# Kernel optimization log

Measured on AMD Instinct MI355X. Metric: run time of the kernel, lower is better.

## Reference

```python
import jax, jax.numpy as jnp
import numpy as np

DIM = 1024
HEADS = 16
HEAD_DIM = DIM // HEADS
FEAT = 256
B, N = 4, 4096


def setup_inputs() -> dict:
    key = jax.random.key(0)
    ks = jax.random.split(key, 10)
    s = 1.0 / np.sqrt(DIM)
    return {
        "x": jax.random.normal(ks[0], (B, N, DIM), jnp.float32),
        "Wq": jax.random.normal(ks[1], (DIM, DIM), jnp.float32) * s,
        "bq": jnp.zeros((DIM,), jnp.float32),
        "Wk": jax.random.normal(ks[2], (DIM, DIM), jnp.float32) * s,
        "bk": jnp.zeros((DIM,), jnp.float32),
        "Wv": jax.random.normal(ks[3], (DIM, DIM), jnp.float32) * s,
        "bv": jnp.zeros((DIM,), jnp.float32),
        "Wo": jax.random.normal(ks[4], (DIM, DIM), jnp.float32) * s,
        "bo": jnp.zeros((DIM,), jnp.float32),
        "random_features": jax.random.normal(ks[5], (HEAD_DIM, FEAT), jnp.float32) / np.sqrt(FEAT),
    }


def reference(x, Wq, bq, Wk, bk, Wv, bv, Wo, bo, random_features):
    Bsz, Nlen, C = x.shape
    # linear projections, reshape to (B, N, H, head_dim)
    q = (x @ Wq + bq).reshape(Bsz, Nlen, HEADS, HEAD_DIM)
    k = (x @ Wk + bk).reshape(Bsz, Nlen, HEADS, HEAD_DIM)
    v = (x @ Wv + bv).reshape(Bsz, Nlen, HEADS, HEAD_DIM)
    # positive feature map: elu(x)+1
    q = jax.nn.elu(q) + 1.0
    k = jax.nn.elu(k) + 1.0
    # random-feature projection (B, N, H, F)
    q = jnp.einsum('bnhd,df->bnhf', q, random_features)
    k = jnp.einsum('bnhd,df->bnhf', k, random_features)
    # kernelized linear attention (no normalization, non-causal as in source)
    kv = jnp.einsum('bnhf,bnhd->bhfd', k, v)          # (B, H, F, head_dim)
    out = jnp.einsum('bnhf,bhfd->bnhd', q, kv)        # (B, N, H, head_dim)
    out = out.reshape(Bsz, Nlen, C)
    return out @ Wo + bo
```

## Files before the change

### kernel.cpp

```cpp
#include <hip/hip_runtime.h>
#include <hip/hip_bf16.h>
#include <cstdint>
#include <cstddef>

using bf16 = __hip_bfloat16;
typedef __attribute__((ext_vector_type(8))) __bf16 bf16x8;
typedef __attribute__((ext_vector_type(4))) float f32x4;

typedef const __attribute__((address_space(1))) void CGV;
typedef __attribute__((address_space(3))) void LDSV;

__device__ __forceinline__ void gload_lds16(const void* g, void* l) {
    __builtin_amdgcn_global_load_lds((CGV*)g, (LDSV*)l, 16, 0, 0);
}

__device__ __forceinline__ float bits2f(unsigned short u) {
    return __uint_as_float(((unsigned)u) << 16);
}
__device__ __forceinline__ unsigned short f2bits(float f) {
    return __builtin_bit_cast(unsigned short, __float2bfloat16(f));
}

__global__ void cast_f32_bf16(const float4* __restrict__ in, ushort4* __restrict__ out, int n4) {
    int i = blockIdx.x * 256 + threadIdx.x;
    if (i < n4) {
        float4 f = in[i];
        ushort4 u;
        u.x = f2bits(f.x); u.y = f2bits(f.y); u.z = f2bits(f.z); u.w = f2bits(f.w);
        out[i] = u;
    }
}

__global__ void transpose_cast(const float* __restrict__ A, const float* __restrict__ B,
                               const float* __restrict__ C, bf16* __restrict__ Wt3) {
    const float* W = (blockIdx.z == 0) ? A : (blockIdx.z == 1) ? B : C;
    bf16* O = Wt3 + (size_t)blockIdx.z * (1024 * 1024);
    __shared__ float tile[32][33];
    int x = blockIdx.x * 32 + threadIdx.x;
    int y0 = blockIdx.y * 32;
    for (int i = threadIdx.y; i < 32; i += 8)
        tile[i][threadIdx.x] = W[(size_t)(y0 + i) * 1024 + x];
    __syncthreads();
    int xo = blockIdx.y * 32 + threadIdx.x;
    int yo = blockIdx.x * 32;
    for (int i = threadIdx.y; i < 32; i += 8)
        O[(size_t)(yo + i) * 1024 + xo] = __float2bfloat16(tile[threadIdx.x][i]);
}

__global__ void g_kernel(const float* __restrict__ RF, float* __restrict__ G) {
    int o = blockIdx.x * 256 + threadIdx.x;
    int i = o >> 6, j = o & 63;
    const float4* a = (const float4*)(RF + (size_t)i * 256);
    const float4* b = (const float4*)(RF + (size_t)j * 256);
    float s = 0.f;
    for (int f = 0; f < 64; f++) {
        float4 x = a[f], y = b[f];
        s += x.x * y.x + x.y * y.y + x.z * y.z + x.w * y.w;
    }
    G[o] = s;
}

__global__ __launch_bounds__(256, 2) void gemm_qkv(
    const bf16* __restrict__ X, const bf16* __restrict__ Wt3,
    const float* __restrict__ bq, const float* __restrict__ bk, const float* __restrict__ bv,
    bf16* __restrict__ Qo, bf16* __restrict__ Ko, bf16* __restrict__ Vo)
{
    __shared__ bf16 As[128 * 64];
    __shared__ bf16 Bs[128 * 64];
    const int z = blockIdx.z;
    const int lid = blockIdx.x + (blockIdx.y << 3);
    const int xcd = lid & 7, seq = lid >> 3;
    const int m0 = (xcd * 16 + (seq >> 3)) * 128;
    const int n0 = (seq & 7) * 128;
    const int tid = threadIdx.x;
    const int w = tid >> 6, lane = tid & 63;
    const int lr = lane >> 3, lc = lane & 7;
    const int sc = lc ^ lr;
    const bf16* Wt = Wt3 + (size_t)z * (1024 * 1024);

    const bf16* ag = X  + (size_t)(m0 + w * 32 + lr) * 1024 + sc * 8;
    const bf16* bg = Wt + (size_t)(n0 + w * 32 + lr) * 1024 + sc * 8;
    bf16* al = As + (w * 32) * 64;
    bf16* bl = Bs + (w * 32) * 64;

    f32x4 acc[4][4];
#pragma unroll
    for (int i = 0; i < 4; i++)
#pragma unroll
        for (int j = 0; j < 4; j++) acc[i][j] = (f32x4){0.f, 0.f, 0.f, 0.f};

    const int lm = lane & 15, quad = lane >> 4;
    const int x0 = (quad ^ (lm & 7)) * 8;
    const int x1 = ((quad + 4) ^ (lm & 7)) * 8;
    const bf16* Ab = As + ((w >> 1) * 64 + lm) * 64;
    const bf16* Bb = Bs + ((w & 1) * 64 + lm) * 64;

    for (int k0 = 0; k0 < 1024; k0 += 64) {
#pragma unroll
        for (int j = 0; j < 4; j++) {
            gload_lds16(ag + (size_t)j * 8 * 1024 + k0, al + j * 8 * 64);
            gload_lds16(bg + (size_t)j * 8 * 1024 + k0, bl + j * 8 * 64);
        }
        __syncthreads();
#pragma unroll
        for (int kk = 0; kk < 2; kk++) {
            const int xo = kk ? x1 : x0;
            bf16x8 a[4], b[4];
#pragma unroll
            for (int i = 0; i < 4; i++) a[i] = *(const bf16x8*)(Ab + i * 16 * 64 + xo);
#pragma unroll
            for (int i = 0; i < 4; i++) b[i] = *(const bf16x8*)(Bb + i * 16 * 64 + xo);
#pragma unroll
            for (int mi = 0; mi < 4; mi++)
#pragma unroll
                for (int ni = 0; ni < 4; ni++)
                    acc[mi][ni] = __builtin_amdgcn_mfma_f32_16x16x32_bf16(
                        a[mi], b[ni], acc[mi][ni], 0, 0, 0);
        }
        __syncthreads();
    }

    const int wr = (w >> 1) * 64, wc = (w & 1) * 64;
    if (z == 0) {
#pragma unroll
        for (int ni = 0; ni < 4; ni++) {
            int col = n0 + wc + ni * 16 + lm;
            float bs = bq[col];
#pragma unroll
            for (int mi = 0; mi < 4; mi++) {
                int row0 = m0 + wr + mi * 16 + quad * 4;
#pragma unroll
                for (int r = 0; r < 4; r++) {
                    float v = acc[mi][ni][r] + bs;
                    v = (v > 0.f) ? (v + 1.f) : __expf(v);
                    Qo[(size_t)(row0 + r) * 1024 + col] = __float2bfloat16(v);
                }
            }
        }
    } else {
        const float* bias = (z == 1) ? bk : bv;
        bf16* Out = (z == 1) ? Ko : Vo;
#pragma unroll
        for (int ni = 0; ni < 4; ni++) {
            int col = n0 + wc + ni * 16 + lm;
            float bs = bias[col];
            int h = col >> 6, d = col & 63;
#pragma unroll
            for (int mi = 0; mi < 4; mi++) {
                int row0 = m0 + wr + mi * 16 + quad * 4;
#pragma unroll
                for (int r = 0; r < 4; r++) {
                    int row = row0 + r;
                    int b = row >> 12, n = row & 4095;
                    float v = acc[mi][ni][r] + bs;
                    if (z == 1) v = (v > 0.f) ? (v + 1.f) : __expf(v);
                    Out[(((size_t)(b * 16 + h) * 4096 + n) << 6) + d] = __float2bfloat16(v);
                }
            }
        }
    }
}

__global__ __launch_bounds__(256, 2) void s_kernel(const bf16* __restrict__ Kp,
                                                   const bf16* __restrict__ Vp,
                                                   float* __restrict__ Spart)
{
    __shared__ bf16 Ks[256 * 64];
    __shared__ bf16 Vs[256 * 64];
    const int bh = blockIdx.x, sp = blockIdx.y;
    const int t = threadIdx.x;
    const int w = t >> 6, lane = t & 63;
    const int eb = (t >> 4) * 4, db = (t & 15) * 4;
    const size_t base = ((size_t)bh * 4096 + sp * 512) * 64;

    float acc[4][4];
#pragma unroll
    for (int i = 0; i < 4; i++)
#pragma unroll
        for (int j = 0; j < 4; j++) acc[i][j] = 0.f;

    const unsigned short* ks = (const unsigned short*)Ks;
    const unsigned short* vs = (const unsigned short*)Vs;

    for (int tile = 0; tile < 2; tile++) {
        const bf16* kg = Kp + base + tile * (256 * 64) + (size_t)w * 4096 + lane * 8;
        const bf16* vg = Vp + base + tile * (256 * 64) + (size_t)w * 4096 + lane * 8;
#pragma unroll
        for (int r = 0; r < 8; r++) {
            gload_lds16(kg + r * 512, Ks + w * 4096 + r * 512);
            gload_lds16(vg + r * 512, Vs + w * 4096 + r * 512);
        }
        __syncthreads();
#pragma unroll 4
        for (int n = 0; n < 256; n++) {
            ushort4 ku = *(const ushort4*)(ks + n * 64 + eb);
            ushort4 vu = *(const ushort4*)(vs + n * 64 + db);
            float kf[4] = {bits2f(ku.x), bits2f(ku.y), bits2f(ku.z), bits2f(ku.w)};
            float vf[4] = {bits2f(vu.x), bits2f(vu.y), bits2f(vu.z), bits2f(vu.w)};
#pragma unroll
            for (int i = 0; i < 4; i++)
#pragma unroll
                for (int j = 0; j < 4; j++) acc[i][j] += kf[i] * vf[j];
        }
        __syncthreads();
    }

    float* spb = Spart + ((size_t)sp * 64 + bh) * 4096;
#pragma unroll
    for (int i = 0; i < 4; i++)
#pragma unroll
        for (int j = 0; j < 4; j++) spb[(eb + i) * 64 + db + j] = acc[i][j];
}

__global__ void reduce_s(const float* __restrict__ Spart, float* __restrict__ S) {
    int bh = blockIdx.x, t = threadIdx.x;
    for (int v = 0; v < 4; v++) {
        int idx = v * 1024 + t * 4;
        float4 a = {0.f, 0.f, 0.f, 0.f};
        for (int s2 = 0; s2 < 8; s2++) {
            float4 p = *(const float4*)&Spart[((size_t)s2 * 64 + bh) * 4096 + idx];
            a.x += p.x; a.y += p.y; a.z += p.z; a.w += p.w;
        }
        *(float4*)&S[(size_t)bh * 4096 + idx] = a;
    }
}

__global__ __launch_bounds__(256) void m_kernel(const float* __restrict__ S,
                                                const float* __restrict__ G,
                                                float* __restrict__ M)
{
    __shared__ float Sl[4096];
    int bh = blockIdx.x, t = threadIdx.x;
    for (int i = t; i < 4096; i += 256) Sl[i] = S[(size_t)bh * 4096 + i];
    __syncthreads();
    int e = t >> 2, d0 = (t & 3) * 16;
    float acc[16];
#pragma unroll
    for (int j = 0; j < 16; j++) acc[j] = 0.f;
    for (int ep = 0; ep < 64; ep++) {
        float g = G[e * 64 + ep];
#pragma unroll
        for (int j = 0; j < 16; j++) acc[j] += g * Sl[ep * 64 + d0 + j];
    }
#pragma unroll
    for (int j = 0; j < 16; j++) M[(size_t)bh * 4096 + e * 64 + d0 + j] = acc[j];
}

__global__ __launch_bounds__(256) void fold_kernel(const float* __restrict__ M,
                                                   const float* __restrict__ Wo,
                                                   bf16* __restrict__ Wo2t)
{
    int x = blockIdx.x;
    int b = x >> 6, h = (x >> 2) & 15, cb = x & 3;
    __shared__ float Ml[4096];
    int t = threadIdx.x;
    for (int i = t; i < 4096; i += 256) {
        int e = i >> 6, d = i & 63;
        Ml[d * 64 + e] = M[((size_t)b * 16 + h) * 4096 + i];
    }
    __syncthreads();
    int c = cb * 256 + t;
    float acc[64];
#pragma unroll
    for (int e = 0; e < 64; e++) acc[e] = 0.f;
    for (int d = 0; d < 64; d++) {
        float wo = Wo[(size_t)(h * 64 + d) * 1024 + c];
#pragma unroll
        for (int e = 0; e < 64; e++) acc[e] += Ml[d * 64 + e] * wo;
    }
    unsigned* outp = (unsigned*)(Wo2t + ((size_t)b * 1024 + c) * 1024 + h * 64);
#pragma unroll
    for (int e = 0; e < 64; e += 2) {
        unsigned lo = f2bits(acc[e]);
        unsigned hi = f2bits(acc[e + 1]);
        outp[e >> 1] = lo | (hi << 16);
    }
}

__global__ __launch_bounds__(256, 2) void gemm_out(
    const bf16* __restrict__ Qp, const bf16* __restrict__ Wo2t,
    const float* __restrict__ bo, float* __restrict__ Out)
{
    __shared__ bf16 As[128 * 64];
    __shared__ bf16 Bs[128 * 64];
    const int lid = blockIdx.x + (blockIdx.y << 3);
    const int xcd = lid & 7, seq = lid >> 3;
    const int m0 = (xcd * 16 + (seq >> 3)) * 128;
    const int n0 = (seq & 7) * 128;
    const int tid = threadIdx.x;
    const int w = tid >> 6, lane = tid & 63;
    const int lr = lane >> 3, lc = lane & 7;
    const int sc = lc ^ lr;
    const bf16* Wt = Wo2t + (size_t)(m0 >> 12) * (1024 * 1024);

    const bf16* ag = Qp + (size_t)(m0 + w * 32 + lr) * 1024 + sc * 8;
    const bf16* bg = Wt + (size_t)(n0 + w * 32 + lr) * 1024 + sc * 8;
    bf16* al = As + (w * 32) * 64;
    bf16* bl = Bs + (w * 32) * 64;

    f32x4 acc[4][4];
#pragma unroll
    for (int i = 0; i < 4; i++)
#pragma unroll
        for (int j = 0; j < 4; j++) acc[i][j] = (f32x4){0.f, 0.f, 0.f, 0.f};

    const int lm = lane & 15, quad = lane >> 4;
    const int x0 = (quad ^ (lm & 7)) * 8;
    const int x1 = ((quad + 4) ^ (lm & 7)) * 8;
    const bf16* Ab = As + ((w >> 1) * 64 + lm) * 64;
    const bf16* Bb = Bs + ((w & 1) * 64 + lm) * 64;

    for (int k0 = 0; k0 < 1024; k0 += 64) {
#pragma unroll
        for (int j = 0; j < 4; j++) {
            gload_lds16(ag + (size_t)j * 8 * 1024 + k0, al + j * 8 * 64);
            gload_lds16(bg + (size_t)j * 8 * 1024 + k0, bl + j * 8 * 64);
        }
        __syncthreads();
#pragma unroll
        for (int kk = 0; kk < 2; kk++) {
            const int xo = kk ? x1 : x0;
            bf16x8 a[4], b[4];
#pragma unroll
            for (int i = 0; i < 4; i++) a[i] = *(const bf16x8*)(Ab + i * 16 * 64 + xo);
#pragma unroll
            for (int i = 0; i < 4; i++) b[i] = *(const bf16x8*)(Bb + i * 16 * 64 + xo);
#pragma unroll
            for (int mi = 0; mi < 4; mi++)
#pragma unroll
                for (int ni = 0; ni < 4; ni++)
                    acc[mi][ni] = __builtin_amdgcn_mfma_f32_16x16x32_bf16(
                        a[mi], b[ni], acc[mi][ni], 0, 0, 0);
        }
        __syncthreads();
    }

    const int wr = (w >> 1) * 64, wc = (w & 1) * 64;
#pragma unroll
    for (int ni = 0; ni < 4; ni++) {
        int col = n0 + wc + ni * 16 + lm;
        float bs = bo[col];
#pragma unroll
        for (int mi = 0; mi < 4; mi++) {
            int row0 = m0 + wr + mi * 16 + quad * 4;
#pragma unroll
            for (int r = 0; r < 4; r++)
                Out[(size_t)(row0 + r) * 1024 + col] = acc[mi][ni][r] + bs;
        }
    }
}

extern "C" void kernel_launch(void* const* d_in, const int* in_sizes, int n_in,
                              void* d_out, int out_size, void* d_ws, size_t ws_size,
                              hipStream_t stream) {
    const float* x  = (const float*)d_in[0];
    const float* Wq = (const float*)d_in[1];
    const float* bq = (const float*)d_in[2];
    const float* Wk = (const float*)d_in[3];
    const float* bk = (const float*)d_in[4];
    const float* Wv = (const float*)d_in[5];
    const float* bv = (const float*)d_in[6];
    const float* Wo = (const float*)d_in[7];
    const float* bo = (const float*)d_in[8];
    const float* RF = (const float*)d_in[9];
    float* out = (float*)d_out;

    char* ws = (char*)d_ws;
    bf16*  Xb    = (bf16*) (ws);
    bf16*  Qp    = (bf16*) (ws + ((size_t)32  << 20));
    bf16*  Kp    = (bf16*) (ws + ((size_t)64  << 20));
    bf16*  Vp    = (bf16*) (ws + ((size_t)96  << 20));
    bf16*  Wt3   = (bf16*) (ws + ((size_t)128 << 20));
    bf16*  Wo2t  = (bf16*) (ws + ((size_t)134 << 20));
    float* Spart = (float*)(ws + ((size_t)142 << 20));
    float* S     = (float*)(ws + ((size_t)150 << 20));
    float* Mm    = (float*)(ws + ((size_t)151 << 20));
    float* G     = (float*)(ws + ((size_t)152 << 20));

    cast_f32_bf16<<<16384, 256, 0, stream>>>((const float4*)x, (ushort4*)Xb, 4194304);
    transpose_cast<<<dim3(32, 32, 3), dim3(32, 8), 0, stream>>>(Wq, Wk, Wv, Wt3);
    g_kernel<<<16, 256, 0, stream>>>(RF, G);
    gemm_qkv<<<dim3(8, 128, 3), 256, 0, stream>>>(Xb, Wt3, bq, bk, bv, Qp, Kp, Vp);
    s_kernel<<<dim3(64, 8), 256, 0, stream>>>(Kp, Vp, Spart);
    reduce_s<<<64, 256, 0, stream>>>(Spart, S);
    m_kernel<<<64, 256, 0, stream>>>(S, G, Mm);
    fold_kernel<<<256, 256, 0, stream>>>(Mm, Wo, Wo2t);
    gemm_out<<<dim3(8, 128), 256, 0, stream>>>(Qp, Wo2t, bo, out);
}
```

Baseline: 394.4 us.

## Merge prep kernels and fuse reduce/M/fold; raise GEMM occupancy hint

Three small preprocessing kernels (input cast, weight transpose-cast, RF Gram) are combined into one launch dispatched by block index. The split-S reduction, M computation and Wo fold are fused into one kernel, so each of its blocks redoes the Spart reduction and G multiply that the separate kernels did once. This removes launch gaps and intermediate global round-trips at the cost of redundant work. The QKV and output GEMM launch bounds change from 2 to 4 blocks per CU, which may constrain registers.

```diff
diff --git a/kernel.cpp b/kernel.cpp
--- a/kernel.cpp
+++ b/kernel.cpp
@@ -21,46 +21,53 @@
     return __builtin_bit_cast(unsigned short, __float2bfloat16(f));
 }
 
-__global__ void cast_f32_bf16(const float4* __restrict__ in, ushort4* __restrict__ out, int n4) {
-    int i = blockIdx.x * 256 + threadIdx.x;
-    if (i < n4) {
-        float4 f = in[i];
+__global__ __launch_bounds__(256) void prep_kernel(
+    const float4* __restrict__ x4, ushort4* __restrict__ Xb4,
+    const float* __restrict__ Wq, const float* __restrict__ Wk,
+    const float* __restrict__ Wv, bf16* __restrict__ Wt3,
+    const float* __restrict__ RF, float* __restrict__ G)
+{
+    const int bi = blockIdx.x;
+    const int t = threadIdx.x;
+    if (bi < 16384) {
+        int i = bi * 256 + t;
+        float4 f = x4[i];
         ushort4 u;
         u.x = f2bits(f.x); u.y = f2bits(f.y); u.z = f2bits(f.z); u.w = f2bits(f.w);
-        out[i] = u;
-    }
-}
-
-__global__ void transpose_cast(const float* __restrict__ A, const float* __restrict__ B,
-                               const float* __restrict__ C, bf16* __restrict__ Wt3) {
-    const float* W = (blockIdx.z == 0) ? A : (blockIdx.z == 1) ? B : C;
-    bf16* O = Wt3 + (size_t)blockIdx.z * (1024 * 1024);
-    __shared__ float tile[32][33];
-    int x = blockIdx.x * 32 + threadIdx.x;
-    int y0 = blockIdx.y * 32;
-    for (int i = threadIdx.y; i < 32; i += 8)
-        tile[i][threadIdx.x] = W[(size_t)(y0 + i) * 1024 + x];
-    __syncthreads();
-    int xo = blockIdx.y * 32 + threadIdx.x;
-    int yo = blockIdx.x * 32;
-    for (int i = threadIdx.y; i < 32; i += 8)
-        O[(size_t)(yo + i) * 1024 + xo] = __float2bfloat16(tile[threadIdx.x][i]);
-}
-
-__global__ void g_kernel(const float* __restrict__ RF, float* __restrict__ G) {
-    int o = blockIdx.x * 256 + threadIdx.x;
-    int i = o >> 6, j = o & 63;
-    const float4* a = (const float4*)(RF + (size_t)i * 256);
-    const float4* b = (const float4*)(RF + (size_t)j * 256);
-    float s = 0.f;
-    for (int f = 0; f < 64; f++) {
-        float4 x = a[f], y = b[f];
-        s += x.x * y.x + x.y * y.y + x.z * y.z + x.w * y.w;
-    }
-    G[o] = s;
-}
-
-__global__ __launch_bounds__(256, 2) void gemm_qkv(
+        Xb4[i] = u;
+    } else if (bi < 19456) {
+        int rem = bi - 16384;
+        int z = rem >> 10;
+        int r2 = rem & 1023;
+        int bx = r2 & 31, by = r2 >> 5;
+        const float* W = (z == 0) ? Wq : (z == 1) ? Wk : Wv;
+        bf16* O = Wt3 + (size_t)z * (1024 * 1024);
+        __shared__ float tile[32][33];
+        int tx = t & 31, ty = t >> 5;
+        int xg = bx * 32 + tx;
+        int y0 = by * 32;
+        for (int i = ty; i < 32; i += 8)
+            tile[i][tx] = W[(size_t)(y0 + i) * 1024 + xg];
+        __syncthreads();
+        int xo = by * 32 + tx;
+        int yo = bx * 32;
+        for (int i = ty; i < 32; i += 8)
+            O[(size_t)(yo + i) * 1024 + xo] = __float2bfloat16(tile[tx][i]);
+    } else {
+        int o = (bi - 19456) * 256 + t;
+        int i = o >> 6, j = o & 63;
+        const float4* a = (const float4*)(RF + (size_t)i * 256);
+        const float4* b = (const float4*)(RF + (size_t)j * 256);
+        float s = 0.f;
+        for (int f = 0; f < 64; f++) {
+            float4 xx = a[f], yy = b[f];
+            s += xx.x * yy.x + xx.y * yy.y + xx.z * yy.z + xx.w * yy.w;
+        }
+        G[o] = s;
+    }
+}
+
+__global__ __launch_bounds__(256, 4) void gemm_qkv(
     const bf16* __restrict__ X, const bf16* __restrict__ Wt3,
     const float* __restrict__ bq, const float* __restrict__ bk, const float* __restrict__ bv,
     bf16* __restrict__ Qo, bf16* __restrict__ Ko, bf16* __restrict__ Vo)
@@ -212,54 +219,44 @@
         for (int j = 0; j < 4; j++) spb[(eb + i) * 64 + db + j] = acc[i][j];
 }
 
-__global__ void reduce_s(const float* __restrict__ Spart, float* __restrict__ S) {
-    int bh = blockIdx.x, t = threadIdx.x;
-    for (int v = 0; v < 4; v++) {
-        int idx = v * 1024 + t * 4;
-        float4 a = {0.f, 0.f, 0.f, 0.f};
-        for (int s2 = 0; s2 < 8; s2++) {
-            float4 p = *(const float4*)&Spart[((size_t)s2 * 64 + bh) * 4096 + idx];
-            a.x += p.x; a.y += p.y; a.z += p.z; a.w += p.w;
-        }
-        *(float4*)&S[(size_t)bh * 4096 + idx] = a;
-    }
-}
-
-__global__ __launch_bounds__(256) void m_kernel(const float* __restrict__ S,
-                                                const float* __restrict__ G,
-                                                float* __restrict__ M)
+__global__ __launch_bounds__(256) void fold2_kernel(const float* __restrict__ Spart,
+                                                    const float* __restrict__ G,
+                                                    const float* __restrict__ Wo,
+                                                    bf16* __restrict__ Wo2t)
 {
     __shared__ float Sl[4096];
-    int bh = blockIdx.x, t = threadIdx.x;
-    for (int i = t; i < 4096; i += 256) Sl[i] = S[(size_t)bh * 4096 + i];
+    __shared__ float Ml[4096];
+    const int xb = blockIdx.x;
+    const int b = xb >> 6, h = (xb >> 2) & 15, cb = xb & 3;
+    const int bh = b * 16 + h;
+    const int t = threadIdx.x;
+
+    for (int i = t; i < 4096; i += 256) {
+        float s = 0.f;
+#pragma unroll
+        for (int sp = 0; sp < 8; sp++)
+            s += Spart[((size_t)sp * 64 + bh) * 4096 + i];
+        Sl[i] = s;
+    }
     __syncthreads();
-    int e = t >> 2, d0 = (t & 3) * 16;
-    float acc[16];
-#pragma unroll
-    for (int j = 0; j < 16; j++) acc[j] = 0.f;
-    for (int ep = 0; ep < 64; ep++) {
-        float g = G[e * 64 + ep];
-#pragma unroll
-        for (int j = 0; j < 16; j++) acc[j] += g * Sl[ep * 64 + d0 + j];
-    }
-#pragma unroll
-    for (int j = 0; j < 16; j++) M[(size_t)bh * 4096 + e * 64 + d0 + j] = acc[j];
-}
-
-__global__ __launch_bounds__(256) void fold_kernel(const float* __restrict__ M,
-                                                   const float* __restrict__ Wo,
-                                                   bf16* __restrict__ Wo2t)
-{
-    int x = blockIdx.x;
-    int b = x >> 6, h = (x >> 2) & 15, cb = x & 3;
-    __shared__ float Ml[4096];
-    int t = threadIdx.x;
-    for (int i = t; i < 4096; i += 256) {
-        int e = i >> 6, d = i & 63;
-        Ml[d * 64 + e] = M[((size_t)b * 16 + h) * 4096 + i];
+
+    {
+        const int e = t >> 2, dblk = (t & 3) * 16;
+        float acc[16];
+#pragma unroll
+        for (int j = 0; j < 16; j++) acc[j] = 0.f;
+        for (int ep = 0; ep < 64; ep++) {
+            float g = G[e * 64 + ep];
+#pragma unroll
+            for (int j = 0; j < 16; j++) acc[j] += g * Sl[ep * 64 + dblk + j];
+        }
+        __syncthreads();
+#pragma unroll
+        for (int j = 0; j < 16; j++) Ml[(dblk + j) * 64 + e] = acc[j];
     }
     __syncthreads();
-    int c = cb * 256 + t;
+
+    const int c = cb * 256 + t;
     float acc[64];
 #pragma unroll
     for (int e = 0; e < 64; e++) acc[e] = 0.f;
@@ -277,7 +274,7 @@
     }
 }
 
-__global__ __launch_bounds__(256, 2) void gemm_out(
+__global__ __launch_bounds__(256, 4) void gemm_out(
     const bf16* __restrict__ Qp, const bf16* __restrict__ Wo2t,
     const float* __restrict__ bo, float* __restrict__ Out)
 {
@@ -373,17 +370,12 @@
     bf16*  Wt3   = (bf16*) (ws + ((size_t)128 << 20));
     bf16*  Wo2t  = (bf16*) (ws + ((size_t)134 << 20));
     float* Spart = (float*)(ws + ((size_t)142 << 20));
-    float* S     = (float*)(ws + ((size_t)150 << 20));
-    float* Mm    = (float*)(ws + ((size_t)151 << 20));
     float* G     = (float*)(ws + ((size_t)152 << 20));
 
-    cast_f32_bf16<<<16384, 256, 0, stream>>>((const float4*)x, (ushort4*)Xb, 4194304);
-    transpose_cast<<<dim3(32, 32, 3), dim3(32, 8), 0, stream>>>(Wq, Wk, Wv, Wt3);
-    g_kernel<<<16, 256, 0, stream>>>(RF, G);
+    prep_kernel<<<19472, 256, 0, stream>>>((const float4*)x, (ushort4*)Xb,
+                                           Wq, Wk, Wv, Wt3, RF, G);
     gemm_qkv<<<dim3(8, 128, 3), 256, 0, stream>>>(Xb, Wt3, bq, bk, bv, Qp, Kp, Vp);
     s_kernel<<<dim3(64, 8), 256, 0, stream>>>(Kp, Vp, Spart);
-    reduce_s<<<64, 256, 0, stream>>>(Spart, S);
-    m_kernel<<<64, 256, 0, stream>>>(S, G, Mm);
-    fold_kernel<<<256, 256, 0, stream>>>(Mm, Wo, Wo2t);
+    fold2_kernel<<<256, 256, 0, stream>>>(Spart, G, Wo, Wo2t);
     gemm_out<<<dim3(8, 128), 256, 0, stream>>>(Qp, Wo2t, bo, out);
 }
```

Measured after the change: 379.8 us. -3.7%, faster.
